# Kernel optimization log

Hardware: AMD Instinct MI355X
Metric: run time of the kernel (lower is better)

The kernel has to match this reference:

```python
import jax, jax.numpy as jnp
import numpy as np

B, N, D, H = 32, 2048, 1024, 16
HD = D // H


def setup_inputs() -> dict:
    key = jax.random.key(0)
    ks = jax.random.split(key, 12)
    s = 1.0 / np.sqrt(D)  # xavier-ish scale for square projections
    return {
        "z": jax.random.normal(ks[0], (B, N, D), dtype=jnp.float32),
        "mask": jax.random.bernoulli(ks[1], 0.9, (B, N)),
        "query": jax.random.normal(ks[2], (1, 1, D), dtype=jnp.float32) * s,
        "w_q": jax.random.normal(ks[3], (D, D), dtype=jnp.float32) * s,
        "w_k": jax.random.normal(ks[4], (D, D), dtype=jnp.float32) * s,
        "w_v": jax.random.normal(ks[5], (D, D), dtype=jnp.float32) * s,
        "b_q": jnp.zeros((D,), dtype=jnp.float32),
        "b_k": jnp.zeros((D,), dtype=jnp.float32),
        "b_v": jnp.zeros((D,), dtype=jnp.float32),
        "w_o": jax.random.normal(ks[6], (D, D), dtype=jnp.float32) * s,
        "b_o": jnp.zeros((D,), dtype=jnp.float32),
    }


def reference(z, mask, query, w_q, w_k, w_v, b_q, b_k, b_v, w_o, b_o):
    # mask: True = valid key. Guarantee at least one valid key per row
    # (torch code sets mask[b, 0] = True for all-False rows).
    all_false = ~jnp.any(mask, axis=1)                 # [B]
    valid = mask.at[:, 0].set(mask[:, 0] | all_false)  # [B, N]

    # Projections (PyTorch Linear: x @ W.T + b)
    q = (query @ w_q.T + b_q).reshape(H, HD)           # single shared query -> [H, HD]
    k = (z @ w_k.T + b_k).reshape(B, N, H, HD)
    v = (z @ w_v.T + b_v).reshape(B, N, H, HD)

    scale = 1.0 / jnp.sqrt(jnp.asarray(HD, dtype=z.dtype))
    scores = jnp.einsum('hd,bnhd->bhn', q, k) * scale  # [B, H, N]
    scores = jnp.where(valid[:, None, :], scores, -jnp.inf)
    attn = jax.nn.softmax(scores, axis=-1)             # [B, H, N]

    pooled = jnp.einsum('bhn,bnhd->bhd', attn, v).reshape(B, D)
    return pooled @ w_o.T + b_o                        # [B, D]
```

## Files before the change

### kernel.cpp

```cpp
#include <hip/hip_runtime.h>
#include <hip/hip_bf16.h>
#include <stdint.h>

#define B_ 32
#define N_ 2048
#define D_ 1024
#define H_ 16

#define NT 16
#define RPAD 1028

typedef __attribute__((ext_vector_type(8))) short short8;
typedef __attribute__((ext_vector_type(4))) float f32x4;

__device__ __forceinline__ unsigned short f2bf(float x) {
    unsigned u = __float_as_uint(x);
    u += 0x7FFFu + ((u >> 16) & 1u);
    return (unsigned short)(u >> 16);
}

__device__ __forceinline__ short8 cvt8(float4 a, float4 b) {
    union { __hip_bfloat162 h[4]; short8 s; } u;
    u.h[0] = __float22bfloat162_rn(make_float2(a.x, a.y));
    u.h[1] = __float22bfloat162_rn(make_float2(a.z, a.w));
    u.h[2] = __float22bfloat162_rn(make_float2(b.x, b.y));
    u.h[3] = __float22bfloat162_rn(make_float2(b.z, b.w));
    return u.s;
}

__global__ __launch_bounds__(256) void prep_q(const float* __restrict__ query,
        const float* __restrict__ w_q, const float* __restrict__ b_q,
        const int* __restrict__ mask, float* __restrict__ q_ws,
        int* __restrict__ any_ws) {
    __shared__ __align__(16) float qv[1024];
    __shared__ float qp[16][17];
    __shared__ int wf[4];
    int bx = blockIdx.x, t = threadIdx.x;
    if (bx < 64) {
        int h = bx >> 2, jg = bx & 3;
        *(float4*)&qv[4 * t] = *(const float4*)&query[4 * t];
        __syncthreads();
        int jl = t >> 4, sub = t & 15;
        int j = h * 64 + jg * 16 + jl;
        const float4* wq4 = (const float4*)(w_q + (size_t)j * 1024);
        const float4* qv4 = (const float4*)qv;
        float a = 0.f;
        #pragma unroll
        for (int kk = 0; kk < 16; kk++) {
            float4 wv = wq4[sub * 16 + kk];
            float4 vv = qv4[sub * 16 + kk];
            a += wv.x * vv.x + wv.y * vv.y + wv.z * vv.z + wv.w * vv.w;
        }
        qp[jl][sub] = a;
        __syncthreads();
        if (sub == 0) {
            float s = 0.f;
            #pragma unroll
            for (int k2 = 0; k2 < 16; k2++) s += qp[jl][k2];
            q_ws[j] = s + b_q[j];
        }
    } else {
        int b = bx - 64;
        int v = 0;
        for (int k = 0; k < 8; k++) v |= mask[b * N_ + k * 256 + t];
        unsigned long long bal = __ballot(v != 0);
        int w = t >> 6;
        if ((t & 63) == 0) wf[w] = (bal != 0ull) ? 1 : 0;
        __syncthreads();
        if (t == 0) any_ws[b] = wf[0] | wf[1] | wf[2] | wf[3];
    }
}

__global__ __launch_bounds__(256) void prep_r(const float* __restrict__ q_ws,
        const float* __restrict__ w_k, unsigned short* __restrict__ rAf) {
    __shared__ float qh[64];
    int bx = blockIdx.x, t = threadIdx.x;
    int h = bx >> 2, dg = bx & 3;
    if (t < 64) qh[t] = q_ws[h * 64 + t];
    __syncthreads();
    int d = dg * 256 + t;
    float acc = 0.f;
    #pragma unroll 4
    for (int j = 0; j < 64; j++)
        acc += qh[j] * w_k[(size_t)(h * 64 + j) * 1024 + d];
    acc *= 0.125f;
    int i = d >> 5, fq = (d >> 3) & 3, jj = d & 7;
    int lane = (fq << 4) | h;
    rAf[(size_t)(i * 64 + lane) * 8 + jj] = f2bf(acc);
}

__global__ __launch_bounds__(256, 1) void main_k(const float* __restrict__ z,
        const int* __restrict__ mask, const int* __restrict__ any_ws,
        const unsigned short* __restrict__ rAf,
        float* __restrict__ part, float* __restrict__ l_part) {
    __shared__ __align__(16) float zt[2][16 * RPAD];
    __shared__ __align__(16) float Ew[4][16][16];
    int bx = blockIdx.x, t = threadIdx.x;
    int b = bx >> 3, c = bx & 7;
    int n0 = c * 256;
    int w = t >> 6, l = t & 63;
    int frow = l & 15, fquad = l >> 4;
    int anyb = any_ws[b];

    short8 rA[32];
    {
        const short8* rA8 = (const short8*)rAf;
        #pragma unroll
        for (int i = 0; i < 32; i++) rA[i] = rA8[i * 64 + l];
    }
    const float* zb = z + (size_t)b * N_ * D_ + n0 * D_;

    float4 ctx[16];
    #pragma unroll
    for (int h = 0; h < 16; h++) ctx[h] = make_float4(0.f, 0.f, 0.f, 0.f);
    float l4[4] = {0.f, 0.f, 0.f, 0.f};

    #define STAGE(p, tile)                                                        \
        {                                                                         \
            const float* gsrc = zb + (size_t)(tile) * 16 * D_ + w * 256 + l * 4;  \
            float* ldst = &zt[(p)][w * 256];                                      \
            _Pragma("unroll")                                                     \
            for (int r = 0; r < 16; r++) {                                        \
                __builtin_amdgcn_global_load_lds(                                 \
                    (const __attribute__((address_space(1))) unsigned int*)       \
                        (gsrc + (size_t)r * D_),                                  \
                    (__attribute__((address_space(3))) unsigned int*)             \
                        (ldst + r * RPAD),                                        \
                    16, 0, 0);                                                    \
            }                                                                     \
        }

    STAGE(0, 0)
    __syncthreads();

    for (int it = 0; it < NT; it++) {
        int p = it & 1;
        if (it + 1 < NT) STAGE(p ^ 1, it + 1)

        f32x4 a0 = {0.f,0.f,0.f,0.f}, a1 = {0.f,0.f,0.f,0.f};
        f32x4 a2 = {0.f,0.f,0.f,0.f}, a3 = {0.f,0.f,0.f,0.f};
        const float* brow = &zt[p][frow * RPAD + fquad * 8];
        #pragma unroll
        for (int i = 0; i < 32; i += 4) {
            float4 z00 = *(const float4*)(brow + (i + 0) * 32);
            float4 z01 = *(const float4*)(brow + (i + 0) * 32 + 4);
            float4 z10 = *(const float4*)(brow + (i + 1) * 32);
            float4 z11 = *(const float4*)(brow + (i + 1) * 32 + 4);
            float4 z20 = *(const float4*)(brow + (i + 2) * 32);
            float4 z21 = *(const float4*)(brow + (i + 2) * 32 + 4);
            float4 z30 = *(const float4*)(brow + (i + 3) * 32);
            float4 z31 = *(const float4*)(brow + (i + 3) * 32 + 4);
            a0 = __builtin_amdgcn_mfma_f32_16x16x32_bf16(rA[i + 0], cvt8(z00, z01), a0, 0, 0, 0);
            a1 = __builtin_amdgcn_mfma_f32_16x16x32_bf16(rA[i + 1], cvt8(z10, z11), a1, 0, 0, 0);
            a2 = __builtin_amdgcn_mfma_f32_16x16x32_bf16(rA[i + 2], cvt8(z20, z21), a2, 0, 0, 0);
            a3 = __builtin_amdgcn_mfma_f32_16x16x32_bf16(rA[i + 3], cvt8(z30, z31), a3, 0, 0, 0);
        }
        f32x4 acc = a0 + a1 + a2 + a3;

        {
            int gn = n0 + it * 16 + frow;
            bool valid = (mask[b * N_ + gn] != 0) || (gn == 0 && anyb == 0);
            float e0 = valid ? __expf(acc[0]) : 0.f;
            float e1 = valid ? __expf(acc[1]) : 0.f;
            float e2 = valid ? __expf(acc[2]) : 0.f;
            float e3 = valid ? __expf(acc[3]) : 0.f;
            l4[0] += e0; l4[1] += e1; l4[2] += e2; l4[3] += e3;
            *(float4*)&Ew[w][frow][fquad * 4] = make_float4(e0, e1, e2, e3);
        }

        {
            const float* zcol = &zt[p][w * 256 + 4 * l];
            #pragma unroll 4
            for (int r = 0; r < 16; r++) {
                float4 zr = *(const float4*)(zcol + r * RPAD);
                const float4* er4 = (const float4*)&Ew[w][r][0];
                float4 e0 = er4[0], e1 = er4[1], e2 = er4[2], e3 = er4[3];
                ctx[0].x  += e0.x * zr.x; ctx[0].y  += e0.x * zr.y; ctx[0].z  += e0.x * zr.z; ctx[0].w  += e0.x * zr.w;
                ctx[1].x  += e0.y * zr.x; ctx[1].y  += e0.y * zr.y; ctx[1].z  += e0.y * zr.z; ctx[1].w  += e0.y * zr.w;
                ctx[2].x  += e0.z * zr.x; ctx[2].y  += e0.z * zr.y; ctx[2].z  += e0.z * zr.z; ctx[2].w  += e0.z * zr.w;
                ctx[3].x  += e0.w * zr.x; ctx[3].y  += e0.w * zr.y; ctx[3].z  += e0.w * zr.z; ctx[3].w  += e0.w * zr.w;
                ctx[4].x  += e1.x * zr.x; ctx[4].y  += e1.x * zr.y; ctx[4].z  += e1.x * zr.z; ctx[4].w  += e1.x * zr.w;
                ctx[5].x  += e1.y * zr.x; ctx[5].y  += e1.y * zr.y; ctx[5].z  += e1.y * zr.z; ctx[5].w  += e1.y * zr.w;
                ctx[6].x  += e1.z * zr.x; ctx[6].y  += e1.z * zr.y; ctx[6].z  += e1.z * zr.z; ctx[6].w  += e1.z * zr.w;
                ctx[7].x  += e1.w * zr.x; ctx[7].y  += e1.w * zr.y; ctx[7].z  += e1.w * zr.z; ctx[7].w  += e1.w * zr.w;
                ctx[8].x  += e2.x * zr.x; ctx[8].y  += e2.x * zr.y; ctx[8].z  += e2.x * zr.z; ctx[8].w  += e2.x * zr.w;
                ctx[9].x  += e2.y * zr.x; ctx[9].y  += e2.y * zr.y; ctx[9].z  += e2.y * zr.z; ctx[9].w  += e2.y * zr.w;
                ctx[10].x += e2.z * zr.x; ctx[10].y += e2.z * zr.y; ctx[10].z += e2.z * zr.z; ctx[10].w += e2.z * zr.w;
                ctx[11].x += e2.w * zr.x; ctx[11].y += e2.w * zr.y; ctx[11].z += e2.w * zr.z; ctx[11].w += e2.w * zr.w;
                ctx[12].x += e3.x * zr.x; ctx[12].y += e3.x * zr.y; ctx[12].z += e3.x * zr.z; ctx[12].w += e3.x * zr.w;
                ctx[13].x += e3.y * zr.x; ctx[13].y += e3.y * zr.y; ctx[13].z += e3.y * zr.z; ctx[13].w += e3.y * zr.w;
                ctx[14].x += e3.z * zr.x; ctx[14].y += e3.z * zr.y; ctx[14].z += e3.z * zr.z; ctx[14].w += e3.z * zr.w;
                ctx[15].x += e3.w * zr.x; ctx[15].y += e3.w * zr.y; ctx[15].z += e3.w * zr.z; ctx[15].w += e3.w * zr.w;
            }
        }
        __syncthreads();
    }

    {
        float* pp = part + (size_t)bx * 16 * 1024 + w * 256 + 4 * l;
        #pragma unroll
        for (int h = 0; h < 16; h++)
            *(float4*)(pp + h * 1024) = ctx[h];
    }
    if (w == 0) {
        #pragma unroll
        for (int r = 0; r < 4; r++) {
            float v = l4[r];
            v += __shfl_xor(v, 1, 64);
            v += __shfl_xor(v, 2, 64);
            v += __shfl_xor(v, 4, 64);
            v += __shfl_xor(v, 8, 64);
            if (frow == 0) l_part[bx * 16 + fquad * 4 + r] = v;
        }
    }
}

__global__ __launch_bounds__(256) void gemv_wv_k(const float* __restrict__ part,
        const float* __restrict__ l_part, const float* __restrict__ w_v,
        const float* __restrict__ b_v, float* __restrict__ pooled) {
    __shared__ __align__(16) float vlds[1024];
    int bx = blockIdx.x, t = threadIdx.x;
    int b = bx >> 4, h = bx & 15;
    float L = 0.f;
    #pragma unroll
    for (int cc = 0; cc < 8; cc++) L += l_part[(b * 8 + cc) * 16 + h];
    float rL = 1.f / L;
    float sx = 0.f, sy = 0.f, sz = 0.f, sw = 0.f;
    #pragma unroll
    for (int cc = 0; cc < 8; cc++) {
        const float4* p4 = (const float4*)&part[(((size_t)(b * 8 + cc)) * 16 + h) * 1024];
        float4 v = p4[t];
        sx += v.x; sy += v.y; sz += v.z; sw += v.w;
    }
    *(float4*)&vlds[4 * t] = make_float4(sx * rL, sy * rL, sz * rL, sw * rL);
    __syncthreads();
    int w = t >> 6, l = t & 63;
    const float4* v4 = (const float4*)vlds;
    float* orow = pooled + (size_t)b * 1024;
    #pragma unroll
    for (int s0 = 0; s0 < 16; s0 += 4) {
        int jb = h * 64 + w * 16 + s0;
        float a0 = 0.f, a1 = 0.f, a2 = 0.f, a3 = 0.f;
        #pragma unroll
        for (int kk = 0; kk < 4; kk++) {
            float4 v = v4[kk * 64 + l];
            float4 w0 = *(const float4*)&w_v[(size_t)(jb + 0) * 1024 + (kk * 64 + l) * 4];
            float4 w1 = *(const float4*)&w_v[(size_t)(jb + 1) * 1024 + (kk * 64 + l) * 4];
            float4 w2 = *(const float4*)&w_v[(size_t)(jb + 2) * 1024 + (kk * 64 + l) * 4];
            float4 w3 = *(const float4*)&w_v[(size_t)(jb + 3) * 1024 + (kk * 64 + l) * 4];
            a0 += w0.x * v.x + w0.y * v.y + w0.z * v.z + w0.w * v.w;
            a1 += w1.x * v.x + w1.y * v.y + w1.z * v.z + w1.w * v.w;
            a2 += w2.x * v.x + w2.y * v.y + w2.z * v.z + w2.w * v.w;
            a3 += w3.x * v.x + w3.y * v.y + w3.z * v.z + w3.w * v.w;
        }
        #pragma unroll
        for (int m = 32; m >= 1; m >>= 1) {
            a0 += __shfl_xor(a0, m, 64); a1 += __shfl_xor(a1, m, 64);
            a2 += __shfl_xor(a2, m, 64); a3 += __shfl_xor(a3, m, 64);
        }
        if (l == 0) {
            orow[jb + 0] = a0 + b_v[jb + 0];
            orow[jb + 1] = a1 + b_v[jb + 1];
            orow[jb + 2] = a2 + b_v[jb + 2];
            orow[jb + 3] = a3 + b_v[jb + 3];
        }
    }
}

__global__ __launch_bounds__(256) void gemv_wo_k(const float* __restrict__ pooled,
        const float* __restrict__ w_o, const float* __restrict__ b_o,
        float* __restrict__ out) {
    __shared__ __align__(16) float vlds[1024];
    int bx = blockIdx.x, t = threadIdx.x;
    int b = bx >> 4, q = bx & 15;
    *(float4*)&vlds[4 * t] = *(const float4*)&pooled[(size_t)b * 1024 + 4 * t];
    __syncthreads();
    int w = t >> 6, l = t & 63;
    const float4* v4 = (const float4*)vlds;
    float* orow = out + (size_t)b * 1024;
    #pragma unroll
    for (int s0 = 0; s0 < 16; s0 += 4) {
        int jb = q * 64 + w * 16 + s0;
        float a0 = 0.f, a1 = 0.f, a2 = 0.f, a3 = 0.f;
        #pragma unroll
        for (int kk = 0; kk < 4; kk++) {
            float4 v = v4[kk * 64 + l];
            float4 w0 = *(const float4*)&w_o[(size_t)(jb + 0) * 1024 + (kk * 64 + l) * 4];
            float4 w1 = *(const float4*)&w_o[(size_t)(jb + 1) * 1024 + (kk * 64 + l) * 4];
            float4 w2 = *(const float4*)&w_o[(size_t)(jb + 2) * 1024 + (kk * 64 + l) * 4];
            float4 w3 = *(const float4*)&w_o[(size_t)(jb + 3) * 1024 + (kk * 64 + l) * 4];
            a0 += w0.x * v.x + w0.y * v.y + w0.z * v.z + w0.w * v.w;
            a1 += w1.x * v.x + w1.y * v.y + w1.z * v.z + w1.w * v.w;
            a2 += w2.x * v.x + w2.y * v.y + w2.z * v.z + w2.w * v.w;
            a3 += w3.x * v.x + w3.y * v.y + w3.z * v.z + w3.w * v.w;
        }
        #pragma unroll
        for (int m = 32; m >= 1; m >>= 1) {
            a0 += __shfl_xor(a0, m, 64); a1 += __shfl_xor(a1, m, 64);
            a2 += __shfl_xor(a2, m, 64); a3 += __shfl_xor(a3, m, 64);
        }
        if (l == 0) {
            orow[jb + 0] = a0 + b_o[jb + 0];
            orow[jb + 1] = a1 + b_o[jb + 1];
            orow[jb + 2] = a2 + b_o[jb + 2];
            orow[jb + 3] = a3 + b_o[jb + 3];
        }
    }
}

extern "C" void kernel_launch(void* const* d_in, const int* in_sizes, int n_in,
                              void* d_out, int out_size, void* d_ws, size_t ws_size,
                              hipStream_t stream) {
    const float* z     = (const float*)d_in[0];
    const int*   mask  = (const int*)d_in[1];
    const float* query = (const float*)d_in[2];
    const float* w_q   = (const float*)d_in[3];
    const float* w_k   = (const float*)d_in[4];
    const float* w_v   = (const float*)d_in[5];
    const float* b_q   = (const float*)d_in[6];
    const float* b_v   = (const float*)d_in[8];
    const float* w_o   = (const float*)d_in[9];
    const float* b_o   = (const float*)d_in[10];
    float* out = (float*)d_out;

    char* ws = (char*)d_ws;
    unsigned short* rAf    = (unsigned short*)(ws + 0);
    float*          q_ws   = (float*)(ws + 32768);
    int*            any_ws = (int*)(ws + 36864);
    float*          l_part = (float*)(ws + 40960);
    float*          pooled = (float*)(ws + 65536);
    float*          part   = (float*)(ws + 1048576);

    prep_q<<<96, 256, 0, stream>>>(query, w_q, b_q, mask, q_ws, any_ws);
    prep_r<<<64, 256, 0, stream>>>(q_ws, w_k, rAf);
    main_k<<<256, 256, 0, stream>>>(z, mask, any_ws, rAf, part, l_part);
    gemv_wv_k<<<512, 256, 0, stream>>>(part, l_part, w_v, b_v, pooled);
    gemv_wo_k<<<512, 256, 0, stream>>>(pooled, w_o, b_o, out);
}
```

Measured before the change: 460.2 us.

## Fuse query and key-projection prep kernels and store partial contexts in bf16

```diff
diff --git a/kernel.cpp b/kernel.cpp
--- a/kernel.cpp
+++ b/kernel.cpp
@@ -18,6 +18,7 @@
     u += 0x7FFFu + ((u >> 16) & 1u);
     return (unsigned short)(u >> 16);
 }
+__device__ __forceinline__ float bflo(unsigned u) { return __uint_as_float(u << 16); }
 
 __device__ __forceinline__ short8 cvt8(float4 a, float4 b) {
     union { __hip_bfloat162 h[4]; short8 s; } u;
@@ -28,37 +29,45 @@
     return u.s;
 }
 
-__global__ __launch_bounds__(256) void prep_q(const float* __restrict__ query,
+__global__ __launch_bounds__(256) void prep_k(const float* __restrict__ query,
         const float* __restrict__ w_q, const float* __restrict__ b_q,
-        const int* __restrict__ mask, float* __restrict__ q_ws,
-        int* __restrict__ any_ws) {
+        const float* __restrict__ w_k, const int* __restrict__ mask,
+        unsigned short* __restrict__ rAf, int* __restrict__ any_ws) {
     __shared__ __align__(16) float qv[1024];
-    __shared__ float qp[16][17];
+    __shared__ float qp[64][5];
+    __shared__ float qh[64];
     __shared__ int wf[4];
     int bx = blockIdx.x, t = threadIdx.x;
     if (bx < 64) {
-        int h = bx >> 2, jg = bx & 3;
+        int h = bx >> 2, dg = bx & 3;
         *(float4*)&qv[4 * t] = *(const float4*)&query[4 * t];
         __syncthreads();
-        int jl = t >> 4, sub = t & 15;
-        int j = h * 64 + jg * 16 + jl;
-        const float4* wq4 = (const float4*)(w_q + (size_t)j * 1024);
-        const float4* qv4 = (const float4*)qv;
-        float a = 0.f;
-        #pragma unroll
-        for (int kk = 0; kk < 16; kk++) {
-            float4 wv = wq4[sub * 16 + kk];
-            float4 vv = qv4[sub * 16 + kk];
-            a += wv.x * vv.x + wv.y * vv.y + wv.z * vv.z + wv.w * vv.w;
-        }
-        qp[jl][sub] = a;
-        __syncthreads();
-        if (sub == 0) {
-            float s = 0.f;
-            #pragma unroll
-            for (int k2 = 0; k2 < 16; k2++) s += qp[jl][k2];
-            q_ws[j] = s + b_q[j];
-        }
+        {
+            int j = t >> 2, sub = t & 3;
+            const float4* wq4 = (const float4*)(w_q + (size_t)(h * 64 + j) * 1024);
+            const float4* qv4 = (const float4*)qv;
+            float a = 0.f;
+            #pragma unroll 8
+            for (int kk = 0; kk < 64; kk++) {
+                float4 wv = wq4[sub * 64 + kk];
+                float4 vv = qv4[sub * 64 + kk];
+                a += wv.x * vv.x + wv.y * vv.y + wv.z * vv.z + wv.w * vv.w;
+            }
+            qp[j][sub] = a;
+        }
+        __syncthreads();
+        if (t < 64)
+            qh[t] = qp[t][0] + qp[t][1] + qp[t][2] + qp[t][3] + b_q[h * 64 + t];
+        __syncthreads();
+        int d = dg * 256 + t;
+        float acc = 0.f;
+        #pragma unroll 8
+        for (int j = 0; j < 64; j++)
+            acc += qh[j] * w_k[(size_t)(h * 64 + j) * 1024 + d];
+        acc *= 0.125f;
+        int i = d >> 5, fq = (d >> 3) & 3, jj = d & 7;
+        int lane = (fq << 4) | h;
+        rAf[(size_t)(i * 64 + lane) * 8 + jj] = f2bf(acc);
     } else {
         int b = bx - 64;
         int v = 0;
@@ -71,28 +80,10 @@
     }
 }
 
-__global__ __launch_bounds__(256) void prep_r(const float* __restrict__ q_ws,
-        const float* __restrict__ w_k, unsigned short* __restrict__ rAf) {
-    __shared__ float qh[64];
-    int bx = blockIdx.x, t = threadIdx.x;
-    int h = bx >> 2, dg = bx & 3;
-    if (t < 64) qh[t] = q_ws[h * 64 + t];
-    __syncthreads();
-    int d = dg * 256 + t;
-    float acc = 0.f;
-    #pragma unroll 4
-    for (int j = 0; j < 64; j++)
-        acc += qh[j] * w_k[(size_t)(h * 64 + j) * 1024 + d];
-    acc *= 0.125f;
-    int i = d >> 5, fq = (d >> 3) & 3, jj = d & 7;
-    int lane = (fq << 4) | h;
-    rAf[(size_t)(i * 64 + lane) * 8 + jj] = f2bf(acc);
-}
-
 __global__ __launch_bounds__(256, 1) void main_k(const float* __restrict__ z,
         const int* __restrict__ mask, const int* __restrict__ any_ws,
         const unsigned short* __restrict__ rAf,
-        float* __restrict__ part, float* __restrict__ l_part) {
+        unsigned short* __restrict__ part, float* __restrict__ l_part) {
     __shared__ __align__(16) float zt[2][16 * RPAD];
     __shared__ __align__(16) float Ew[4][16][16];
     int bx = blockIdx.x, t = threadIdx.x;
@@ -197,10 +188,14 @@
     }
 
     {
-        float* pp = part + (size_t)bx * 16 * 1024 + w * 256 + 4 * l;
-        #pragma unroll
-        for (int h = 0; h < 16; h++)
-            *(float4*)(pp + h * 1024) = ctx[h];
+        unsigned short* pp = part + (size_t)bx * 16 * 1024 + w * 256 + 4 * l;
+        #pragma unroll
+        for (int h = 0; h < 16; h++) {
+            ushort4 o;
+            o.x = f2bf(ctx[h].x); o.y = f2bf(ctx[h].y);
+            o.z = f2bf(ctx[h].z); o.w = f2bf(ctx[h].w);
+            *(ushort4*)(pp + h * 1024) = o;
+        }
     }
     if (w == 0) {
         #pragma unroll
@@ -215,7 +210,7 @@
     }
 }
 
-__global__ __launch_bounds__(256) void gemv_wv_k(const float* __restrict__ part,
+__global__ __launch_bounds__(256) void gemv_wv_k(const unsigned short* __restrict__ part,
         const float* __restrict__ l_part, const float* __restrict__ w_v,
         const float* __restrict__ b_v, float* __restrict__ pooled) {
     __shared__ __align__(16) float vlds[1024];
@@ -228,9 +223,9 @@
     float sx = 0.f, sy = 0.f, sz = 0.f, sw = 0.f;
     #pragma unroll
     for (int cc = 0; cc < 8; cc++) {
-        const float4* p4 = (const float4*)&part[(((size_t)(b * 8 + cc)) * 16 + h) * 1024];
-        float4 v = p4[t];
-        sx += v.x; sy += v.y; sz += v.z; sw += v.w;
+        const ushort4* p4 = (const ushort4*)&part[(((size_t)(b * 8 + cc)) * 16 + h) * 1024];
+        ushort4 u = p4[t];
+        sx += bflo(u.x); sy += bflo(u.y); sz += bflo(u.z); sw += bflo(u.w);
     }
     *(float4*)&vlds[4 * t] = make_float4(sx * rL, sy * rL, sz * rL, sw * rL);
     __syncthreads();
@@ -325,14 +320,12 @@
 
     char* ws = (char*)d_ws;
     unsigned short* rAf    = (unsigned short*)(ws + 0);
-    float*          q_ws   = (float*)(ws + 32768);
-    int*            any_ws = (int*)(ws + 36864);
+    int*            any_ws = (int*)(ws + 32768);
     float*          l_part = (float*)(ws + 40960);
     float*          pooled = (float*)(ws + 65536);
-    float*          part   = (float*)(ws + 1048576);
-
-    prep_q<<<96, 256, 0, stream>>>(query, w_q, b_q, mask, q_ws, any_ws);
-    prep_r<<<64, 256, 0, stream>>>(q_ws, w_k, rAf);
+    unsigned short* part   = (unsigned short*)(ws + 1048576);
+
+    prep_k<<<96, 256, 0, stream>>>(query, w_q, b_q, w_k, mask, rAf, any_ws);
     main_k<<<256, 256, 0, stream>>>(z, mask, any_ws, rAf, part, l_part);
     gemv_wv_k<<<512, 256, 0, stream>>>(part, l_part, w_v, b_v, pooled);
     gemv_wo_k<<<512, 256, 0, stream>>>(pooled, w_o, b_o, out);
```

Result: no change. 457.4 us (-0.6%).
